# Kernel tuning notes

Hardware: AMD Instinct MI355X
Metric: run time of the kernel (lower is better)

## Reference

```python
import jax, jax.numpy as jnp
import numpy as np
from jax import lax

B, T, D, H = 64, 2048, 256, 256


def setup_inputs() -> dict:
    key = jax.random.key(0)
    k1, k2, k3 = jax.random.split(key, 3)
    xs = jax.random.normal(k1, (B, T, D), dtype=jnp.float32)
    # scale weights ~ 1/sqrt(fan_in) to keep tanh out of saturation
    W_ih = jax.random.normal(k2, (D, H), dtype=jnp.float32) / np.sqrt(D)
    W_hh = jax.random.normal(k3, (H, H), dtype=jnp.float32) / np.sqrt(H)
    b_hh = jnp.zeros((H,), dtype=jnp.float32)
    c = jnp.zeros((B, H), dtype=jnp.float32)
    return {"c": c, "xs": xs, "W_ih": W_ih, "W_hh": W_hh, "b_hh": b_hh}


def reference(c, xs, W_ih, W_hh, b_hh):
    # Elman RNN: h_t = tanh(x_t @ W_ih + h_{t-1} @ W_hh + b_hh)
    # (the ih bias is created but never applied in the original module)
    # Precompute the input projection for all timesteps in one big GEMM.
    px = jnp.einsum('btd,dh->bth', xs, W_ih)  # [B, T, H]

    def step(h, px_t):
        h_new = jnp.tanh(h @ W_hh + b_hh + px_t)
        return h_new, h_new

    h_final, ys = lax.scan(step, c, px.transpose(1, 0, 2))  # ys: [T, B, H]
    return h_final, ys.transpose(1, 0, 2)  # carry [B,H], outputs [B,T,H]
```

## Files before the change

kernel.cpp:

```cpp
#include <hip/hip_runtime.h>


typedef _Float16 half8 __attribute__((ext_vector_type(8)));
typedef float floatx4 __attribute__((ext_vector_type(4)));
typedef float f32x4 __attribute__((ext_vector_type(4)));

constexpr int Bb = 64, Tt = 2048, Dd = 256, Hh = 256;

__device__ __forceinline__ int lds_addr(int row, int col) {
    return row * 512 + ((((col >> 3) ^ (row & 7)) & 31) << 4) + ((col & 7) << 1);
}

__device__ __forceinline__ float fast_tanh(float x) {
    float e = __builtin_amdgcn_exp2f(x * 2.885390081777927f);
    float r = __builtin_amdgcn_rcpf(e + 1.0f);
    return __builtin_fmaf(-2.0f, r, 1.0f);
}

#define LDS_BARRIER() asm volatile("s_waitcnt lgkmcnt(0)\n\ts_barrier" ::: "memory")

__global__ __launch_bounds__(256, 2) void px_gemm(const float* __restrict__ xs,
                                                  const float* __restrict__ Wih,
                                                  const float* __restrict__ bhh,
                                                  float* __restrict__ px) {
    const int lane = threadIdx.x & 63;
    const int w = threadIdx.x >> 6;
    const int q = lane >> 4;
    const int m = lane & 15;

    half8 bf[4][8];
#pragma unroll
    for (int tt = 0; tt < 4; ++tt) {
        const int n = 64 * w + 16 * tt + m;
#pragma unroll
        for (int c = 0; c < 8; ++c) {
            half8 f;
#pragma unroll
            for (int j = 0; j < 8; ++j)
                f[j] = (_Float16)Wih[(32 * c + 8 * q + j) * Hh + n];
            bf[tt][c] = f;
        }
    }
    float bias[4];
#pragma unroll
    for (int tt = 0; tt < 4; ++tt) bias[tt] = bhh[64 * w + 16 * tt + m];

    for (int i = 0; i < 8; ++i) {
        const int tau = blockIdx.x * 8 + i;
        const float* arow = xs + (size_t)(tau * 16 + m) * Dd;
        half8 af[8];
#pragma unroll
        for (int c = 0; c < 8; ++c) {
            f32x4 lo = *(const f32x4*)(arow + 32 * c + 8 * q);
            f32x4 hi = *(const f32x4*)(arow + 32 * c + 8 * q + 4);
            half8 f;
            f[0] = (_Float16)lo[0]; f[1] = (_Float16)lo[1];
            f[2] = (_Float16)lo[2]; f[3] = (_Float16)lo[3];
            f[4] = (_Float16)hi[0]; f[5] = (_Float16)hi[1];
            f[6] = (_Float16)hi[2]; f[7] = (_Float16)hi[3];
            af[c] = f;
        }
        floatx4 acc[4];
#pragma unroll
        for (int tt = 0; tt < 4; ++tt) {
            acc[tt][0] = bias[tt]; acc[tt][1] = bias[tt];
            acc[tt][2] = bias[tt]; acc[tt][3] = bias[tt];
        }
#pragma unroll
        for (int c = 0; c < 8; ++c)
#pragma unroll
            for (int tt = 0; tt < 4; ++tt)
                acc[tt] = __builtin_amdgcn_mfma_f32_16x16x32_f16(af[c], bf[tt][c], acc[tt], 0, 0, 0);
#pragma unroll
        for (int tt = 0; tt < 4; ++tt)
#pragma unroll
            for (int r = 0; r < 4; ++r)
                px[(size_t)(tau * 16 + 4 * q + r) * Hh + 64 * w + 16 * tt + m] = acc[tt][r];
    }
}

__global__ __launch_bounds__(512, 2) void rnn_scan(const float* __restrict__ c0,
                                                   const float* __restrict__ Whh,
                                                   float* __restrict__ hfin,
                                                   float* __restrict__ ys) {
    __shared__ alignas(16) unsigned char hb[2][8192];
    const int g = blockIdx.x;
    const int lane = threadIdx.x & 63;
    const int w = threadIdx.x >> 6;
    const int q = lane >> 4;
    const int m = lane & 15;

    half8 bf[2][8];
#pragma unroll
    for (int tt = 0; tt < 2; ++tt) {
        const int n = 32 * w + 16 * tt + m;
#pragma unroll
        for (int c = 0; c < 8; ++c) {
            half8 f;
#pragma unroll
            for (int j = 0; j < 8; ++j)
                f[j] = (_Float16)Whh[(32 * c + 8 * q + j) * Hh + n];
            bf[tt][c] = f;
        }
    }

    for (int i = threadIdx.x; i < 16 * 256; i += 512) {
        const int row = i >> 8, col = i & 255;
        *(_Float16*)&hb[0][lds_addr(row, col)] = (_Float16)c0[(16 * g + row) * Hh + col];
    }

    unsigned boff[8];
#pragma unroll
    for (int tt = 0; tt < 2; ++tt)
#pragma unroll
        for (int r = 0; r < 4; ++r)
            boff[4 * tt + r] =
                (unsigned)(((16 * g + 4 * q + r) * Tt) * Hh + 32 * w + 16 * tt + m) * 4u;

    int ard[8];
#pragma unroll
    for (int c = 0; c < 8; ++c)
        ard[c] = m * 512 + ((((4 * c + q) ^ (m & 7)) & 31) << 4);

    int wad[8];
#pragma unroll
    for (int tt = 0; tt < 2; ++tt)
#pragma unroll
        for (int r = 0; r < 4; ++r)
            wad[4 * tt + r] = lds_addr(4 * q + r, 32 * w + 16 * tt + m);

    const char* pxp = (const char*)ys;
    const char* pxlast = (const char*)ys + (size_t)(Tt - 1) * Hh * 4;
    char* yst = (char*)ys;

    floatx4 pxA[2], pxB[2];
#pragma unroll
    for (int k = 0; k < 8; ++k) pxA[k >> 2][k & 3] = *(const float*)(pxp + boff[k]);
    pxp += Hh * 4;

    __syncthreads();

#define RNN_STEP(P, PXC, PXN, LASTCHK, TCUR)                                   \
    {                                                                          \
                                 \
        half8 af[8];                                                           \
        _Pragma("unroll") for (int c2 = 0; c2 < 8; ++c2)                       \
            af[c2] = *(const half8*)&hb[(P)][ard[c2]];                         \
             \
        const char* pf = (pxp > pxlast) ? pxlast : pxp;     \
        _Pragma("unroll") for (int k2 = 0; k2 < 8; ++k2)                       \
            PXN[k2 >> 2][k2 & 3] = *(const float*)(pf + boff[k2]);             \
        pxp += Hh * 4;                                                         \
        floatx4 acc0 = PXC[0], acc1 = PXC[1];                                  \
        _Pragma("unroll") for (int c2 = 0; c2 < 8; ++c2)                       \
            acc0 = __builtin_amdgcn_mfma_f32_16x16x32_f16(af[c2], bf[0][c2],   \
                                                          acc0, 0, 0, 0);      \
        _Pragma("unroll") for (int c2 = 0; c2 < 8; ++c2)                       \
            acc1 = __builtin_amdgcn_mfma_f32_16x16x32_f16(af[c2], bf[1][c2],   \
                                                          acc1, 0, 0, 0);      \
        _Pragma("unroll") for (int r2 = 0; r2 < 4; ++r2) {                     \
            const float hv = fast_tanh(acc0[r2]);                              \
            *(float*)(yst + boff[r2]) = hv;                                    \
            *(_Float16*)&hb[(P) ^ 1][wad[r2]] = (_Float16)hv;                  \
        }                                                                      \
        _Pragma("unroll") for (int r2 = 0; r2 < 4; ++r2) {                     \
            const float hv = fast_tanh(acc1[r2]);                              \
            *(float*)(yst + boff[4 + r2]) = hv;                                \
            *(_Float16*)&hb[(P) ^ 1][wad[4 + r2]] = (_Float16)hv;              \
        }                                                                      \
        if ((LASTCHK) && (TCUR) == Tt - 1) {                                   \
            _Pragma("unroll") for (int u2 = 0; u2 < 2; ++u2)                   \
                _Pragma("unroll") for (int r2 = 0; r2 < 4; ++r2) {             \
                    const floatx4 a2 = (u2 == 0) ? acc0 : acc1;                \
                    hfin[(16 * g + 4 * q + r2) * Hh + 32 * w + 16 * u2 + m] =  \
                        fast_tanh(a2[r2]);                                     \
                }                                                              \
        }                                                                      \
        yst += Hh * 4;                                                         \
        LDS_BARRIER();                                                         \
    }

    for (int t = 0; t < Tt; t += 2) {
        RNN_STEP(0, pxA, pxB, 0, t)
        RNN_STEP(1, pxB, pxA, 1, t + 1)
    }
#undef RNN_STEP
}

extern "C" void kernel_launch(void* const* d_in, const int* in_sizes, int n_in,
                              void* d_out, int out_size, void* d_ws, size_t ws_size,
                              hipStream_t stream) {
    const float* c0  = (const float*)d_in[0];
    const float* xs  = (const float*)d_in[1];
    const float* Wih = (const float*)d_in[2];
    const float* Whh = (const float*)d_in[3];
    const float* bhh = (const float*)d_in[4];
    float* out = (float*)d_out;
    float* hfin = out;
    float* ys = out + Bb * Hh;

    px_gemm<<<1024, 256, 0, stream>>>(xs, Wih, bhh, ys);
    rnn_scan<<<Bb / 16, 512, 0, stream>>>(c0, Whh, hfin, ys);
}
```

Measured before the change: 1.723 ms.

## Split RNN scan across twice as many blocks with 8 batch rows each

The recurrent scan now assigns 8 batch rows per block instead of 16, launching 8 blocks instead of 4. The 16-row MFMA tile is filled by duplicating rows, and only lanes with valid rows write outputs. The serial per-step chain gets shorter because each block handles fewer rows, at the cost of half the MFMA work being wasted. The px GEMM also swaps its MFMA operands so each lane holds contiguous output columns, allowing vectorized 16-byte stores and a vectorized bias load.

Result: slower. 1.863 ms (+8.1%).

```diff
diff --git a/kernel.cpp b/kernel.cpp
--- a/kernel.cpp
+++ b/kernel.cpp
@@ -41,9 +41,10 @@
             bf[tt][c] = f;
         }
     }
-    float bias[4];
-#pragma unroll
-    for (int tt = 0; tt < 4; ++tt) bias[tt] = bhh[64 * w + 16 * tt + m];
+    f32x4 bias2[4];
+#pragma unroll
+    for (int tt = 0; tt < 4; ++tt)
+        bias2[tt] = *(const f32x4*)(bhh + 64 * w + 16 * tt + 4 * q);
 
     for (int i = 0; i < 8; ++i) {
         const int tau = blockIdx.x * 8 + i;
@@ -63,19 +64,18 @@
         floatx4 acc[4];
 #pragma unroll
         for (int tt = 0; tt < 4; ++tt) {
-            acc[tt][0] = bias[tt]; acc[tt][1] = bias[tt];
-            acc[tt][2] = bias[tt]; acc[tt][3] = bias[tt];
+            acc[tt][0] = bias2[tt][0]; acc[tt][1] = bias2[tt][1];
+            acc[tt][2] = bias2[tt][2]; acc[tt][3] = bias2[tt][3];
         }
 #pragma unroll
         for (int c = 0; c < 8; ++c)
 #pragma unroll
             for (int tt = 0; tt < 4; ++tt)
-                acc[tt] = __builtin_amdgcn_mfma_f32_16x16x32_f16(af[c], bf[tt][c], acc[tt], 0, 0, 0);
+                acc[tt] = __builtin_amdgcn_mfma_f32_16x16x32_f16(bf[tt][c], af[c], acc[tt], 0, 0, 0);
 #pragma unroll
         for (int tt = 0; tt < 4; ++tt)
-#pragma unroll
-            for (int r = 0; r < 4; ++r)
-                px[(size_t)(tau * 16 + 4 * q + r) * Hh + 64 * w + 16 * tt + m] = acc[tt][r];
+            *(f32x4*)(px + (size_t)(tau * 16 + m) * Hh + 64 * w + 16 * tt + 4 * q) =
+                *(f32x4*)&acc[tt];
     }
 }
 
@@ -83,7 +83,7 @@
                                                    const float* __restrict__ Whh,
                                                    float* __restrict__ hfin,
                                                    float* __restrict__ ys) {
-    __shared__ alignas(16) unsigned char hb[2][8192];
+    __shared__ alignas(16) unsigned char hb[2][4096];
     const int g = blockIdx.x;
     const int lane = threadIdx.x & 63;
     const int w = threadIdx.x >> 6;
@@ -104,9 +104,9 @@
         }
     }
 
-    for (int i = threadIdx.x; i < 16 * 256; i += 512) {
+    for (int i = threadIdx.x; i < 8 * 256; i += 512) {
         const int row = i >> 8, col = i & 255;
-        *(_Float16*)&hb[0][lds_addr(row, col)] = (_Float16)c0[(16 * g + row) * Hh + col];
+        *(_Float16*)&hb[0][lds_addr(row, col)] = (_Float16)c0[(8 * g + row) * Hh + col];
     }
 
     unsigned boff[8];
@@ -115,27 +115,27 @@
 #pragma unroll
         for (int r = 0; r < 4; ++r)
             boff[4 * tt + r] =
-                (unsigned)(((16 * g + 4 * q + r) * Tt) * Hh + 32 * w + 16 * tt + m) * 4u;
+                (unsigned)(((8 * g + ((4 * q + r) & 7)) * Tt) * Hh + 32 * w + 16 * tt + m) * 4u;
 
     int ard[8];
 #pragma unroll
     for (int c = 0; c < 8; ++c)
-        ard[c] = m * 512 + ((((4 * c + q) ^ (m & 7)) & 31) << 4);
+        ard[c] = (m & 7) * 512 + ((((4 * c + q) ^ (m & 7)) & 31) << 4);
 
     int wad[8];
 #pragma unroll
     for (int tt = 0; tt < 2; ++tt)
 #pragma unroll
         for (int r = 0; r < 4; ++r)
-            wad[4 * tt + r] = lds_addr(4 * q + r, 32 * w + 16 * tt + m);
+            wad[4 * tt + r] = lds_addr((4 * q + r) & 7, 32 * w + 16 * tt + m);
 
     const char* pxp = (const char*)ys;
     const char* pxlast = (const char*)ys + (size_t)(Tt - 1) * Hh * 4;
     char* yst = (char*)ys;
 
-    floatx4 pxA[2], pxB[2];
-#pragma unroll
-    for (int k = 0; k < 8; ++k) pxA[k >> 2][k & 3] = *(const float*)(pxp + boff[k]);
+    float pxA[8], pxB[8];
+#pragma unroll
+    for (int k = 0; k < 8; ++k) pxA[k] = *(const float*)(pxp + boff[k]);
     pxp += Hh * 4;
 
     __syncthreads();
@@ -149,32 +149,33 @@
              \
         const char* pf = (pxp > pxlast) ? pxlast : pxp;     \
         _Pragma("unroll") for (int k2 = 0; k2 < 8; ++k2)                       \
-            PXN[k2 >> 2][k2 & 3] = *(const float*)(pf + boff[k2]);             \
+            PXN[k2] = *(const float*)(pf + boff[k2]);                          \
         pxp += Hh * 4;                                                         \
-        floatx4 acc0 = PXC[0], acc1 = PXC[1];                                  \
+        floatx4 acc0, acc1;                                                    \
+        _Pragma("unroll") for (int i2 = 0; i2 < 4; ++i2) {                     \
+            acc0[i2] = PXC[i2]; acc1[i2] = PXC[4 + i2];                        \
+        }                                                                      \
         _Pragma("unroll") for (int c2 = 0; c2 < 8; ++c2)                       \
             acc0 = __builtin_amdgcn_mfma_f32_16x16x32_f16(af[c2], bf[0][c2],   \
                                                           acc0, 0, 0, 0);      \
         _Pragma("unroll") for (int c2 = 0; c2 < 8; ++c2)                       \
             acc1 = __builtin_amdgcn_mfma_f32_16x16x32_f16(af[c2], bf[1][c2],   \
                                                           acc1, 0, 0, 0);      \
-        _Pragma("unroll") for (int r2 = 0; r2 < 4; ++r2) {                     \
-            const float hv = fast_tanh(acc0[r2]);                              \
-            *(float*)(yst + boff[r2]) = hv;                                    \
-            *(_Float16*)&hb[(P) ^ 1][wad[r2]] = (_Float16)hv;                  \
-        }                                                                      \
-        _Pragma("unroll") for (int r2 = 0; r2 < 4; ++r2) {                     \
-            const float hv = fast_tanh(acc1[r2]);                              \
-            *(float*)(yst + boff[4 + r2]) = hv;                                \
-            *(_Float16*)&hb[(P) ^ 1][wad[4 + r2]] = (_Float16)hv;              \
-        }                                                                      \
-        if ((LASTCHK) && (TCUR) == Tt - 1) {                                   \
-            _Pragma("unroll") for (int u2 = 0; u2 < 2; ++u2)                   \
-                _Pragma("unroll") for (int r2 = 0; r2 < 4; ++r2) {             \
-                    const floatx4 a2 = (u2 == 0) ? acc0 : acc1;                \
-                    hfin[(16 * g + 4 * q + r2) * Hh + 32 * w + 16 * u2 + m] =  \
-                        fast_tanh(a2[r2]);                                     \
-                }                                                              \
+        if (lane < 32) {                 \
+            _Pragma("unroll") for (int r2 = 0; r2 < 4; ++r2) {                 \
+                const float hv = fast_tanh(acc0[r2]);                          \
+                *(float*)(yst + boff[r2]) = hv;                                \
+                *(_Float16*)&hb[(P) ^ 1][wad[r2]] = (_Float16)hv;              \
+                if ((LASTCHK) && (TCUR) == Tt - 1)                             \
+                    hfin[(8 * g + 4 * q + r2) * Hh + 32 * w + m] = hv;         \
+            }                                                                  \
+            _Pragma("unroll") for (int r2 = 0; r2 < 4; ++r2) {                 \
+                const float hv = fast_tanh(acc1[r2]);                          \
+                *(float*)(yst + boff[4 + r2]) = hv;                            \
+                *(_Float16*)&hb[(P) ^ 1][wad[4 + r2]] = (_Float16)hv;          \
+                if ((LASTCHK) && (TCUR) == Tt - 1)                             \
+                    hfin[(8 * g + 4 * q + r2) * Hh + 32 * w + 16 + m] = hv;    \
+            }                                                                  \
         }                                                                      \
         yst += Hh * 4;                                                         \
         LDS_BARRIER();                                                         \
@@ -200,5 +201,5 @@
     float* ys = out + Bb * Hh;
 
     px_gemm<<<1024, 256, 0, stream>>>(xs, Wih, bhh, ys);
-    rnn_scan<<<Bb / 16, 512, 0, stream>>>(c0, Whh, hfin, ys);
-}
+    rnn_scan<<<Bb / 8, 512, 0, stream>>>(c0, Whh, hfin, ys);
+}
```
